# Optimization experiments

Measured on AMD Instinct MI355X. Metric: run time of the kernel, lower is better.

Reference implementation:

```python
import jax, jax.numpy as jnp
import numpy as np

D_MODEL, D_K, D_V = 512, 64, 64
B, S = 8, 4096


def setup_inputs() -> dict:
    key = jax.random.key(0)
    ks = jax.random.split(key, 10)
    scale = 1.0 / np.sqrt(D_MODEL)
    return {
        "q": jax.random.normal(ks[0], (B, S, D_MODEL), dtype=jnp.float32),
        "k": jax.random.normal(ks[1], (B, S, D_MODEL), dtype=jnp.float32),
        "v": jax.random.normal(ks[2], (B, S, D_MODEL), dtype=jnp.float32),
        "mask": jax.random.randint(ks[3], (B, S), 0, 2, dtype=jnp.int32),
        "Wq": jax.random.uniform(ks[4], (D_MODEL, D_K), jnp.float32, -scale, scale),
        "bq": jax.random.uniform(ks[5], (D_K,), jnp.float32, -scale, scale),
        "Wk": jax.random.uniform(ks[6], (D_MODEL, D_K), jnp.float32, -scale, scale),
        "bk": jax.random.uniform(ks[7], (D_K,), jnp.float32, -scale, scale),
        "Wv": jax.random.uniform(ks[8], (D_MODEL, D_V), jnp.float32, -scale, scale),
        "bv": jax.random.uniform(ks[9], (D_V,), jnp.float32, -scale, scale),
    }


def reference(q, k, v, mask, Wq, bq, Wk, bk, Wv, bv):
    # single-head QKV projections
    qh = jnp.einsum("bsd,dk->bsk", q, Wq) + bq  # [B,S,d_k]
    kh = jnp.einsum("bsd,dk->bsk", k, Wk) + bk  # [B,S,d_k]
    vh = jnp.einsum("bsd,dv->bsv", v, Wv) + bv  # [B,S,d_v]
    scores = jnp.einsum("bqk,bsk->bqs", qh, kh) / jnp.sqrt(jnp.float32(D_K))
    # key-padding mask: mask [B,S] -> [B,1,S], masked positions -> -1e10
    scores = jnp.where(mask[:, None, :] == 0, jnp.float32(-1e10), scores)
    attn = jax.nn.softmax(scores, axis=-1)
    return jnp.einsum("bqs,bsv->bqv", attn, vh)
```

## Files before the change

### kernel.cpp

```cpp
#include <hip/hip_runtime.h>

typedef __attribute__((ext_vector_type(8))) short bf16x8;
typedef __attribute__((ext_vector_type(4))) float f32x4;
typedef __attribute__((ext_vector_type(4))) unsigned short u16x4;

__device__ __forceinline__ short f2bf(float f) {
  unsigned int u = __builtin_bit_cast(unsigned int, f);
  u += 0x7fffu + ((u >> 16) & 1u);
  return (short)(u >> 16);
}

__global__ void prep_w(const float* __restrict__ Wq, const float* __restrict__ Wk,
                       const float* __restrict__ Wv, unsigned short* __restrict__ wt) {
  int idx = blockIdx.x * 256 + threadIdx.x;
  int m = idx >> 15;
  int rem = idx & 32767;
  int n = rem >> 9;
  int k = rem & 511;
  const float* W = (m == 0) ? Wq : ((m == 1) ? Wk : Wv);
  wt[idx] = (unsigned short)f2bf(W[k * 64 + n]);
}

__global__ __launch_bounds__(256, 5) void proj_kernel(
    const float* __restrict__ qx, const float* __restrict__ kx, const float* __restrict__ vx,
    const unsigned short* __restrict__ wt, const int* __restrict__ mask,
    const float* __restrict__ bqp, const float* __restrict__ bkp, const float* __restrict__ bvp,
    unsigned short* __restrict__ qo, unsigned short* __restrict__ ko,
    unsigned short* __restrict__ vo) {
  __shared__ unsigned short lds[64 * 256];
  const int mode = blockIdx.y;
  const float* x = (mode == 0) ? qx : ((mode == 1) ? kx : vx);
  const float* bias = (mode == 0) ? bqp : ((mode == 1) ? bkp : bvp);
  const unsigned short* wtm = wt + mode * (64 * 512);
  const float osc = (mode == 0) ? 0.18033688011112042f : 1.0f;

  const int tid = threadIdx.x;
  const int w = tid >> 6, lane = tid & 63;
  const int g = lane >> 4, ln = lane & 15;
  const int rowbase = blockIdx.x * 64;

  const f32x4 fz = {0.f, 0.f, 0.f, 0.f};
  f32x4 acc[4];
#pragma unroll
  for (int nf = 0; nf < 4; ++nf) acc[nf] = fz;

  const float* xrow = x + (size_t)(rowbase + w * 16 + ln) * 512 + g * 8;

  auto stageW = [&](int half) {
#pragma unroll
    for (int i = 0; i < 8; ++i) {
      int c = tid + i * 256;
      int n = c >> 5, kc = c & 31;
      bf16x8 d = *reinterpret_cast<const bf16x8*>(wtm + n * 512 + half * 256 + kc * 8);
      int bo = (n * 512 + kc * 16) ^ ((n & 7) << 4);
      *reinterpret_cast<bf16x8*>(reinterpret_cast<char*>(lds) + bo) = d;
    }
  };

  stageW(0);
  float4 xa = reinterpret_cast<const float4*>(xrow)[0];
  float4 xb = reinterpret_cast<const float4*>(xrow)[1];
  __syncthreads();

#pragma unroll
  for (int t = 0; t < 16; ++t) {
    float4 na, nb;
    if (t < 15) {
      const float4* np = reinterpret_cast<const float4*>(xrow + (t + 1) * 32);
      na = np[0];
      nb = np[1];
    }
    if (t == 8) {
      __syncthreads();
      stageW(1);
      __syncthreads();
    }
    bf16x8 af;
    af[0] = f2bf(xa.x); af[1] = f2bf(xa.y); af[2] = f2bf(xa.z); af[3] = f2bf(xa.w);
    af[4] = f2bf(xb.x); af[5] = f2bf(xb.y); af[6] = f2bf(xb.z); af[7] = f2bf(xb.w);
    int ks = t & 7;
#pragma unroll
    for (int nf = 0; nf < 4; ++nf) {
      int n = nf * 16 + ln;
      int bo = (n * 512 + ks * 64 + g * 16) ^ ((n & 7) << 4);
      bf16x8 bfrag = *reinterpret_cast<const bf16x8*>(reinterpret_cast<const char*>(lds) + bo);
      acc[nf] = __builtin_amdgcn_mfma_f32_16x16x32_bf16(af, bfrag, acc[nf], 0, 0, 0);
    }
    xa = na;
    xb = nb;
  }

  float bc[4];
#pragma unroll
  for (int nf = 0; nf < 4; ++nf) bc[nf] = bias[nf * 16 + ln];

  if (mode < 2) {
    unsigned short* o = (mode == 0) ? qo : ko;
#pragma unroll
    for (int nf = 0; nf < 4; ++nf)
#pragma unroll
      for (int r = 0; r < 4; ++r) {
        int row = rowbase + w * 16 + g * 4 + r;
        o[(size_t)row * 64 + nf * 16 + ln] = (unsigned short)f2bf((acc[nf][r] + bc[nf]) * osc);
      }
  } else {
    __syncthreads();
#pragma unroll
    for (int nf = 0; nf < 4; ++nf)
#pragma unroll
      for (int r = 0; r < 4; ++r) {
        int srow = w * 16 + g * 4 + r;
        lds[srow * 64 + nf * 16 + ln] = (unsigned short)f2bf(acc[nf][r] + bc[nf]);
      }
    __syncthreads();
    int b = rowbase >> 12, s0 = rowbase & 4095;
    int dv = tid & 63, sc = tid >> 6;
#pragma unroll
    for (int i = 0; i < 2; ++i) {
      int sbase = s0 + sc * 16 + i * 8;
      const int* mrow = mask + b * 4096 + sbase;
      bf16x8 pack;
#pragma unroll
      for (int j = 0; j < 8; ++j) {
        short vvv = (short)lds[(sc * 16 + i * 8 + j) * 64 + dv];
        pack[j] = mrow[j] ? vvv : (short)0;
      }
      *reinterpret_cast<bf16x8*>(vo + (size_t)(b * 64 + dv) * 4096 + sbase) = pack;
    }
  }
}

#define KVBLK 128
#define NT 16

__global__ __launch_bounds__(256, 2) void attn_kernel(
    const unsigned short* __restrict__ qh, const unsigned short* __restrict__ kh,
    const unsigned short* __restrict__ vt, const int* __restrict__ mask,
    float* __restrict__ out0, float* __restrict__ out1,
    float* __restrict__ l0p, float* __restrict__ l1p) {
  __shared__ unsigned short kt[2][KVBLK * 64];
  __shared__ unsigned short vv[2][80 * 128];

  const int b = blockIdx.y;
  const int z = blockIdx.z;
  const int kv0 = z * (NT * KVBLK);
  float* __restrict__ optr = z ? out1 : out0;
  float* __restrict__ lptr = z ? l1p : l0p;
  const int qbase = blockIdx.x * 128;
  const int tid = threadIdx.x;
  const int w = tid >> 6, lane = tid & 63;
  const int g = lane >> 4, ln = lane & 15;

  for (int i = tid; i < 15 * 128; i += 256) {
    vv[0][65 * 128 + i] = 0;
    vv[1][65 * 128 + i] = 0;
  }

  bf16x8 qa[2][2];
#pragma unroll
  for (int qf = 0; qf < 2; ++qf) {
    int row = qbase + w * 32 + qf * 16 + ln;
    const unsigned short* qp = qh + (size_t)(b * 4096 + row) * 64;
    qa[qf][0] = *reinterpret_cast<const bf16x8*>(qp + g * 8);
    qa[qf][1] = *reinterpret_cast<const bf16x8*>(qp + 32 + g * 8);
  }

  const f32x4 fz = {0.f, 0.f, 0.f, 0.f};
  f32x4 accO[2][5];
#pragma unroll
  for (int qf = 0; qf < 2; ++qf)
#pragma unroll
    for (int nf = 0; nf < 5; ++nf) accO[qf][nf] = fz;

  const unsigned short* khb = kh + (size_t)b * 4096 * 64;
  const unsigned short* vtb = vt + (size_t)b * 64 * 4096;

  bf16x8 kreg[4], vreg[4];
  int mreg = 0;
  auto issue = [&](int ti) {
    int kvbase = kv0 + ti * KVBLK;
#pragma unroll
    for (int i = 0; i < 4; ++i) {
      int c = tid + i * 256;
      vreg[i] = *reinterpret_cast<const bf16x8*>(vtb + (size_t)(c >> 4) * 4096 + kvbase + (c & 15) * 8);
      kreg[i] = *reinterpret_cast<const bf16x8*>(khb + (size_t)(kvbase + (c >> 3)) * 64 + (c & 7) * 8);
    }
    if (tid < KVBLK) mreg = mask[b * 4096 + kvbase + tid];
  };
  auto commit = [&](int bs) {
#pragma unroll
    for (int i = 0; i < 4; ++i) {
      int c = tid + i * 256;
      int kbo = ((c >> 3) * 128 + (c & 7) * 16) ^ (((c >> 3) & 7) << 4);
      *reinterpret_cast<bf16x8*>(reinterpret_cast<char*>(kt[bs]) + kbo) = kreg[i];
      int dv = c >> 4;
      int P0 = (c & 15) * 8;
      int c2 = P0 >> 5, h = (P0 >> 4) & 1, gg = (P0 >> 2) & 3;
      int x1 = 32 * c2 + 8 * gg + 4 * h;
      int swz = (dv & 7) << 4;
      union { bf16x8 v; u16x4 h4[2]; } sp; sp.v = vreg[i];
      *reinterpret_cast<u16x4*>(reinterpret_cast<char*>(vv[bs]) + ((dv * 256 + 2 * x1) ^ swz)) = sp.h4[0];
      *reinterpret_cast<u16x4*>(reinterpret_cast<char*>(vv[bs]) + ((dv * 256 + 2 * x1 + 16) ^ swz)) = sp.h4[1];
    }
    if (tid < KVBLK) {
      int p = tid;
      int x = 32 * (p >> 5) + 8 * ((p >> 2) & 3) + 4 * ((p >> 4) & 1) + (p & 3);
      vv[bs][64 * 128 + x] = mreg ? (unsigned short)0x3F80 : (unsigned short)0;
    }
  };

  issue(0);
  commit(0);
  __syncthreads();
  int cur = 0;

  for (int ti = 0; ti < NT; ++ti) {
    if (ti + 1 < NT) issue(ti + 1);

    f32x4 s0[8], s1[8];
#pragma unroll
    for (int nf = 0; nf < 8; ++nf) { s0[nf] = fz; s1[nf] = fz; }
    __builtin_amdgcn_s_setprio(1);
#pragma unroll
    for (int c2 = 0; c2 < 2; ++c2)
#pragma unroll
      for (int nf = 0; nf < 8; ++nf) {
        int kvr = nf * 16 + ln;
        int bo = (kvr * 128 + c2 * 64 + g * 16) ^ ((kvr & 7) << 4);
        bf16x8 kf = *reinterpret_cast<const bf16x8*>(reinterpret_cast<const char*>(kt[cur]) + bo);
        s0[nf] = __builtin_amdgcn_mfma_f32_16x16x32_bf16(kf, qa[0][c2], s0[nf], 0, 0, 0);
        s1[nf] = __builtin_amdgcn_mfma_f32_16x16x32_bf16(kf, qa[1][c2], s1[nf], 0, 0, 0);
      }
    __builtin_amdgcn_s_setprio(0);

    unsigned int pw[2][4][4];
#pragma unroll
    for (int c2 = 0; c2 < 4; ++c2)
#pragma unroll
      for (int hh = 0; hh < 2; ++hh) {
        {
          float p0 = __builtin_exp2f(s0[2 * c2 + hh][0]);
          float p1 = __builtin_exp2f(s0[2 * c2 + hh][1]);
          float p2 = __builtin_exp2f(s0[2 * c2 + hh][2]);
          float p3 = __builtin_exp2f(s0[2 * c2 + hh][3]);
          unsigned int w0, w1;
          asm("v_cvt_pk_bf16_f32 %0, %1, %2" : "=v"(w0) : "v"(p0), "v"(p1));
          asm("v_cvt_pk_bf16_f32 %0, %1, %2" : "=v"(w1) : "v"(p2), "v"(p3));
          pw[0][c2][2 * hh] = w0;
          pw[0][c2][2 * hh + 1] = w1;
        }
        {
          float p0 = __builtin_exp2f(s1[2 * c2 + hh][0]);
          float p1 = __builtin_exp2f(s1[2 * c2 + hh][1]);
          float p2 = __builtin_exp2f(s1[2 * c2 + hh][2]);
          float p3 = __builtin_exp2f(s1[2 * c2 + hh][3]);
          unsigned int w0, w1;
          asm("v_cvt_pk_bf16_f32 %0, %1, %2" : "=v"(w0) : "v"(p0), "v"(p1));
          asm("v_cvt_pk_bf16_f32 %0, %1, %2" : "=v"(w1) : "v"(p2), "v"(p3));
          pw[1][c2][2 * hh] = w0;
          pw[1][c2][2 * hh + 1] = w1;
        }
      }

    __builtin_amdgcn_s_setprio(1);
#pragma unroll
    for (int c2 = 0; c2 < 4; ++c2) {
      union { unsigned int u[4]; bf16x8 v; } pa0, pa1;
#pragma unroll
      for (int t = 0; t < 4; ++t) { pa0.u[t] = pw[0][c2][t]; pa1.u[t] = pw[1][c2][t]; }
#pragma unroll
      for (int nf = 0; nf < 5; ++nf) {
        int dvr = nf * 16 + ln;
        int bo = (dvr * 256 + c2 * 64 + g * 16) ^ ((dvr & 7) << 4);
        bf16x8 vb = *reinterpret_cast<const bf16x8*>(reinterpret_cast<const char*>(vv[cur]) + bo);
        accO[0][nf] = __builtin_amdgcn_mfma_f32_16x16x32_bf16(pa0.v, vb, accO[0][nf], 0, 0, 0);
        accO[1][nf] = __builtin_amdgcn_mfma_f32_16x16x32_bf16(pa1.v, vb, accO[1][nf], 0, 0, 0);
      }
    }
    __builtin_amdgcn_s_setprio(0);

    if (ti + 1 < NT) commit(cur ^ 1);
    __syncthreads();
    cur ^= 1;
  }

#pragma unroll
  for (int qf = 0; qf < 2; ++qf)
#pragma unroll
    for (int r = 0; r < 4; ++r) {
      int grow = b * 4096 + qbase + w * 32 + qf * 16 + g * 4 + r;
#pragma unroll
      for (int nf = 0; nf < 4; ++nf)
        optr[(size_t)grow * 64 + nf * 16 + ln] = accO[qf][nf][r];
      if (ln == 0) lptr[grow] = accO[qf][4][r];
    }
}

__global__ __launch_bounds__(256) void combine_kernel(
    float* __restrict__ out, const float* __restrict__ po1,
    const float* __restrict__ l0p, const float* __restrict__ l1p) {
  int idx = blockIdx.x * 256 + threadIdx.x;
  int row = idx >> 4;
  float rl = 1.0f / (l0p[row] + l1p[row]);
  float4 a = reinterpret_cast<float4*>(out)[idx];
  float4 c = reinterpret_cast<const float4*>(po1)[idx];
  a.x = (a.x + c.x) * rl;
  a.y = (a.y + c.y) * rl;
  a.z = (a.z + c.z) * rl;
  a.w = (a.w + c.w) * rl;
  reinterpret_cast<float4*>(out)[idx] = a;
}

extern "C" void kernel_launch(void* const* d_in, const int* in_sizes, int n_in,
                              void* d_out, int out_size, void* d_ws, size_t ws_size,
                              hipStream_t stream) {
  const float* q = (const float*)d_in[0];
  const float* k = (const float*)d_in[1];
  const float* v = (const float*)d_in[2];
  const int* mask = (const int*)d_in[3];
  const float* Wq = (const float*)d_in[4];
  const float* bq = (const float*)d_in[5];
  const float* Wk = (const float*)d_in[6];
  const float* bk = (const float*)d_in[7];
  const float* Wv = (const float*)d_in[8];
  const float* bv = (const float*)d_in[9];

  char* wsb = (char*)d_ws;
  unsigned short* qh = (unsigned short*)(wsb);
  unsigned short* kh = (unsigned short*)(wsb + (4u << 20));
  unsigned short* vt = (unsigned short*)(wsb + (8u << 20));
  unsigned short* wt = (unsigned short*)(wsb + (12u << 20));
  float* po1 = (float*)(wsb + (12u << 20) + 196608);
  float* l0p = (float*)(wsb + (12u << 20) + 196608 + (8u << 20));
  float* l1p = l0p + 32768;

  prep_w<<<384, 256, 0, stream>>>(Wq, Wk, Wv, wt);
  proj_kernel<<<dim3(512, 3), 256, 0, stream>>>(q, k, v, wt, mask, bq, bk, bv, qh, kh, vt);
  attn_kernel<<<dim3(32, 8, 2), 256, 0, stream>>>(qh, kh, vt, mask,
                                                  (float*)d_out, po1, l0p, l1p);
  combine_kernel<<<2048, 256, 0, stream>>>((float*)d_out, po1, l0p, l1p);
}
```

Before: 111.2 us.

## Stage projection inputs through LDS with coalesced loads and halve rows per block

```diff
diff --git a/kernel.cpp b/kernel.cpp
--- a/kernel.cpp
+++ b/kernel.cpp
@@ -21,13 +21,15 @@
   wt[idx] = (unsigned short)f2bf(W[k * 64 + n]);
 }
 
-__global__ __launch_bounds__(256, 5) void proj_kernel(
+__global__ __launch_bounds__(256, 2) void proj_kernel(
     const float* __restrict__ qx, const float* __restrict__ kx, const float* __restrict__ vx,
     const unsigned short* __restrict__ wt, const int* __restrict__ mask,
     const float* __restrict__ bqp, const float* __restrict__ bkp, const float* __restrict__ bvp,
     unsigned short* __restrict__ qo, unsigned short* __restrict__ ko,
     unsigned short* __restrict__ vo) {
-  __shared__ unsigned short lds[64 * 256];
+  __shared__ unsigned short xs[32 * 512];
+  __shared__ unsigned short wl[64 * 256];
+
   const int mode = blockIdx.y;
   const float* x = (mode == 0) ? qx : ((mode == 1) ? kx : vx);
   const float* bias = (mode == 0) ? bqp : ((mode == 1) ? bkp : bvp);
@@ -37,14 +39,8 @@
   const int tid = threadIdx.x;
   const int w = tid >> 6, lane = tid & 63;
   const int g = lane >> 4, ln = lane & 15;
-  const int rowbase = blockIdx.x * 64;
-
-  const f32x4 fz = {0.f, 0.f, 0.f, 0.f};
-  f32x4 acc[4];
-#pragma unroll
-  for (int nf = 0; nf < 4; ++nf) acc[nf] = fz;
-
-  const float* xrow = x + (size_t)(rowbase + w * 16 + ln) * 512 + g * 8;
+  const int rowbase = blockIdx.x * 32;
+  const int rh = w & 1, h = w >> 1;
 
   auto stageW = [&](int half) {
 #pragma unroll
@@ -53,80 +49,92 @@
       int n = c >> 5, kc = c & 31;
       bf16x8 d = *reinterpret_cast<const bf16x8*>(wtm + n * 512 + half * 256 + kc * 8);
       int bo = (n * 512 + kc * 16) ^ ((n & 7) << 4);
-      *reinterpret_cast<bf16x8*>(reinterpret_cast<char*>(lds) + bo) = d;
+      *reinterpret_cast<bf16x8*>(reinterpret_cast<char*>(wl) + bo) = d;
     }
   };
 
+  {
+    const float* src = x + (size_t)rowbase * 512;
+#pragma unroll
+    for (int i = 0; i < 16; ++i) {
+      int idx = i * 256 + tid;
+      float4 d = *reinterpret_cast<const float4*>(src + (size_t)idx * 4);
+      int row = idx >> 7, col4 = idx & 127;
+      u16x4 pk;
+      pk[0] = (unsigned short)f2bf(d.x);
+      pk[1] = (unsigned short)f2bf(d.y);
+      pk[2] = (unsigned short)f2bf(d.z);
+      pk[3] = (unsigned short)f2bf(d.w);
+      int u8 = col4 ^ ((row & 7) << 1);
+      *reinterpret_cast<u16x4*>(reinterpret_cast<char*>(xs) + row * 1024 + u8 * 8) = pk;
+    }
+  }
   stageW(0);
-  float4 xa = reinterpret_cast<const float4*>(xrow)[0];
-  float4 xb = reinterpret_cast<const float4*>(xrow)[1];
   __syncthreads();
 
+  const f32x4 fz = {0.f, 0.f, 0.f, 0.f};
+  f32x4 acc[2];
+  acc[0] = fz;
+  acc[1] = fz;
+
+  const int lrow = rh * 16 + ln;
+  const char* xrow_lds = reinterpret_cast<const char*>(xs) + lrow * 1024;
+  const int c7 = lrow & 7;
+
 #pragma unroll
   for (int t = 0; t < 16; ++t) {
-    float4 na, nb;
-    if (t < 15) {
-      const float4* np = reinterpret_cast<const float4*>(xrow + (t + 1) * 32);
-      na = np[0];
-      nb = np[1];
-    }
     if (t == 8) {
       __syncthreads();
       stageW(1);
       __syncthreads();
     }
-    bf16x8 af;
-    af[0] = f2bf(xa.x); af[1] = f2bf(xa.y); af[2] = f2bf(xa.z); af[3] = f2bf(xa.w);
-    af[4] = f2bf(xb.x); af[5] = f2bf(xb.y); af[6] = f2bf(xb.z); af[7] = f2bf(xb.w);
+    int v = t * 4 + g;
+    bf16x8 af = *reinterpret_cast<const bf16x8*>(xrow_lds + ((v ^ c7) * 16));
     int ks = t & 7;
 #pragma unroll
-    for (int nf = 0; nf < 4; ++nf) {
-      int n = nf * 16 + ln;
+    for (int nfi = 0; nfi < 2; ++nfi) {
+      int n = h * 32 + nfi * 16 + ln;
       int bo = (n * 512 + ks * 64 + g * 16) ^ ((n & 7) << 4);
-      bf16x8 bfrag = *reinterpret_cast<const bf16x8*>(reinterpret_cast<const char*>(lds) + bo);
-      acc[nf] = __builtin_amdgcn_mfma_f32_16x16x32_bf16(af, bfrag, acc[nf], 0, 0, 0);
-    }
-    xa = na;
-    xb = nb;
-  }
-
-  float bc[4];
-#pragma unroll
-  for (int nf = 0; nf < 4; ++nf) bc[nf] = bias[nf * 16 + ln];
+      bf16x8 bfrag = *reinterpret_cast<const bf16x8*>(reinterpret_cast<const char*>(wl) + bo);
+      acc[nfi] = __builtin_amdgcn_mfma_f32_16x16x32_bf16(af, bfrag, acc[nfi], 0, 0, 0);
+    }
+  }
+
+  float bc[2];
+#pragma unroll
+  for (int nfi = 0; nfi < 2; ++nfi) bc[nfi] = bias[h * 32 + nfi * 16 + ln];
 
   if (mode < 2) {
     unsigned short* o = (mode == 0) ? qo : ko;
 #pragma unroll
-    for (int nf = 0; nf < 4; ++nf)
+    for (int nfi = 0; nfi < 2; ++nfi)
 #pragma unroll
       for (int r = 0; r < 4; ++r) {
-        int row = rowbase + w * 16 + g * 4 + r;
-        o[(size_t)row * 64 + nf * 16 + ln] = (unsigned short)f2bf((acc[nf][r] + bc[nf]) * osc);
+        int row = rowbase + rh * 16 + g * 4 + r;
+        o[(size_t)row * 64 + h * 32 + nfi * 16 + ln] =
+            (unsigned short)f2bf((acc[nfi][r] + bc[nfi]) * osc);
       }
   } else {
     __syncthreads();
 #pragma unroll
-    for (int nf = 0; nf < 4; ++nf)
+    for (int nfi = 0; nfi < 2; ++nfi)
 #pragma unroll
       for (int r = 0; r < 4; ++r) {
-        int srow = w * 16 + g * 4 + r;
-        lds[srow * 64 + nf * 16 + ln] = (unsigned short)f2bf(acc[nf][r] + bc[nf]);
+        int srow = rh * 16 + g * 4 + r;
+        xs[srow * 64 + h * 32 + nfi * 16 + ln] = (unsigned short)f2bf(acc[nfi][r] + bc[nfi]);
       }
     __syncthreads();
     int b = rowbase >> 12, s0 = rowbase & 4095;
     int dv = tid & 63, sc = tid >> 6;
-#pragma unroll
-    for (int i = 0; i < 2; ++i) {
-      int sbase = s0 + sc * 16 + i * 8;
-      const int* mrow = mask + b * 4096 + sbase;
-      bf16x8 pack;
-#pragma unroll
-      for (int j = 0; j < 8; ++j) {
-        short vvv = (short)lds[(sc * 16 + i * 8 + j) * 64 + dv];
-        pack[j] = mrow[j] ? vvv : (short)0;
-      }
-      *reinterpret_cast<bf16x8*>(vo + (size_t)(b * 64 + dv) * 4096 + sbase) = pack;
-    }
+    int sbase = s0 + sc * 8;
+    const int* mrow = mask + b * 4096 + sbase;
+    bf16x8 pack;
+#pragma unroll
+    for (int j = 0; j < 8; ++j) {
+      short vvv = (short)xs[(sc * 8 + j) * 64 + dv];
+      pack[j] = mrow[j] ? vvv : (short)0;
+    }
+    *reinterpret_cast<bf16x8*>(vo + (size_t)(b * 64 + dv) * 4096 + sbase) = pack;
   }
 }
 
@@ -195,8 +203,8 @@
       *reinterpret_cast<bf16x8*>(reinterpret_cast<char*>(kt[bs]) + kbo) = kreg[i];
       int dv = c >> 4;
       int P0 = (c & 15) * 8;
-      int c2 = P0 >> 5, h = (P0 >> 4) & 1, gg = (P0 >> 2) & 3;
-      int x1 = 32 * c2 + 8 * gg + 4 * h;
+      int c2 = P0 >> 5, hh = (P0 >> 4) & 1, gg = (P0 >> 2) & 3;
+      int x1 = 32 * c2 + 8 * gg + 4 * hh;
       int swz = (dv & 7) << 4;
       union { bf16x8 v; u16x4 h4[2]; } sp; sp.v = vreg[i];
       *reinterpret_cast<u16x4*>(reinterpret_cast<char*>(vv[bs]) + ((dv * 256 + 2 * x1) ^ swz)) = sp.h4[0];
@@ -204,8 +212,8 @@
     }
     if (tid < KVBLK) {
       int p = tid;
-      int x = 32 * (p >> 5) + 8 * ((p >> 2) & 3) + 4 * ((p >> 4) & 1) + (p & 3);
-      vv[bs][64 * 128 + x] = mreg ? (unsigned short)0x3F80 : (unsigned short)0;
+      int xx = 32 * (p >> 5) + 8 * ((p >> 2) & 3) + 4 * ((p >> 4) & 1) + (p & 3);
+      vv[bs][64 * 128 + xx] = mreg ? (unsigned short)0x3F80 : (unsigned short)0;
     }
   };
 
@@ -335,7 +343,7 @@
   float* l1p = l0p + 32768;
 
   prep_w<<<384, 256, 0, stream>>>(Wq, Wk, Wv, wt);
-  proj_kernel<<<dim3(512, 3), 256, 0, stream>>>(q, k, v, wt, mask, bq, bk, bv, qh, kh, vt);
+  proj_kernel<<<dim3(1024, 3), 256, 0, stream>>>(q, k, v, wt, mask, bq, bk, bv, qh, kh, vt);
   attn_kernel<<<dim3(32, 8, 2), 256, 0, stream>>>(qh, kh, vt, mask,
                                                   (float*)d_out, po1, l0p, l1p);
   combine_kernel<<<2048, 256, 0, stream>>>((float*)d_out, po1, l0p, l1p);
```

Result: no change. 109.8 us (-1.3%).
